# Performance work log

Measured on AMD Instinct MI355X. Metric: run time of the kernel, lower is better.

Reference implementation:

```python
import jax, jax.numpy as jnp
import numpy as np
import math

DIM_EMB = 1024
KSQRT = math.sqrt(DIM_EMB)


def setup_inputs() -> dict:
    key = jax.random.key(0)
    ks = jax.random.split(key, 7)
    b, t, e, d = 4, 4096, DIM_EMB, 1024
    s = 1.0 / math.sqrt(e)
    return {
        "x": jax.random.normal(ks[0], (b, t, e), dtype=jnp.float32),
        "Wq": jax.random.normal(ks[1], (d, e), dtype=jnp.float32) * s,
        "bq": jax.random.normal(ks[2], (d,), dtype=jnp.float32) * s,
        "Wk": jax.random.normal(ks[3], (d, e), dtype=jnp.float32) * s,
        "bk": jax.random.normal(ks[4], (d,), dtype=jnp.float32) * s,
        "Wv": jax.random.normal(ks[5], (d, e), dtype=jnp.float32) * s,
        "bv": jax.random.normal(ks[6], (d,), dtype=jnp.float32) * s,
    }


def reference(x, Wq, bq, Wk, bk, Wv, bv):
    # Linear projections: x [b,t,e] @ W.T [e,d] + b
    q = jnp.einsum('bte,de->btd', x, Wq) + bq
    k = jnp.einsum('bte,de->btd', x, Wk) + bk
    v = jnp.einsum('bte,de->btd', x, Wv) + bv
    # scaled dot-product attention, scale = sqrt(dim_emb) per source
    dot = jnp.einsum('bqd,bkd->bqk', q, k) / KSQRT
    p = jax.nn.softmax(dot, axis=-1)  # dim=2 == last axis for 3D tensor
    z = jnp.einsum('bqk,bkd->bqd', p, v)
    return z
```

## Files before the change

kernel.cpp:

```cpp
#include <hip/hip_runtime.h>
#include <hip/hip_bf16.h>

typedef __bf16 bf16x8 __attribute__((ext_vector_type(8)));
typedef float  f32x4  __attribute__((ext_vector_type(4)));

typedef __attribute__((address_space(1))) const void* as1p;
typedef __attribute__((address_space(3))) void*       as3p;

__device__ __forceinline__ void gl16(const void* g, void* l) {
    __builtin_amdgcn_global_load_lds((as1p)g, (as3p)l, 16, 0, 0);
}
#define MEMFENCE asm volatile("" ::: "memory")
#define BARRIER  do { MEMFENCE; __builtin_amdgcn_s_barrier(); MEMFENCE; } while (0)

__global__ __launch_bounds__(256)
void cvt_f32_bf16(const float* __restrict__ in, __bf16* __restrict__ out, long n8)
{
    long i = (long)blockIdx.x * blockDim.x + threadIdx.x;
    const long stride = (long)gridDim.x * blockDim.x;
    for (; i < n8; i += stride) {
        f32x4 a = ((const f32x4*)in)[2*i];
        f32x4 b = ((const f32x4*)in)[2*i + 1];
        bf16x8 o;
        #pragma unroll
        for (int j = 0; j < 4; ++j) { o[j] = (__bf16)a[j]; o[4+j] = (__bf16)b[j]; }
        ((bf16x8*)out)[i] = o;
    }
}

__global__ __launch_bounds__(256)
void pack_bias(const float* __restrict__ a, const float* __restrict__ b,
               const float* __restrict__ c, float* __restrict__ o)
{
    int i = blockIdx.x * 256 + threadIdx.x;
    const float* s = (i < 1024) ? a : (i < 2048) ? b : c;
    o[i] = s[i & 1023];
}

__global__ __launch_bounds__(256)
void prepass(const float* __restrict__ x,
             const float* __restrict__ Wq, const float* __restrict__ Wk,
             const float* __restrict__ Wv,
             const float* __restrict__ bq, const float* __restrict__ bk,
             const float* __restrict__ bv,
             __bf16* __restrict__ wall, __bf16* __restrict__ xb,
             float* __restrict__ bp)
{
    const long NW8 = 393216;
    const long NX8 = 2097152;
    long tid0 = (long)blockIdx.x * blockDim.x + threadIdx.x;
    if (tid0 < 3072) {
        const float* s = (tid0 < 1024) ? bq : (tid0 < 2048) ? bk : bv;
        bp[tid0] = s[tid0 & 1023];
    }
    const long stride = (long)gridDim.x * blockDim.x;
    for (long i = tid0; i < NW8 + NX8; i += stride) {
        const float* src;
        __bf16* dst;
        if (i < NW8) {
            int w = (int)(i >> 17);
            long off8 = i & 131071;
            src = ((w == 0) ? Wq : (w == 1) ? Wk : Wv) + off8 * 8;
            dst = wall + i * 8;
        } else {
            long j8 = i - NW8;
            src = x + j8 * 8;
            dst = xb + j8 * 8;
        }
        f32x4 a = ((const f32x4*)src)[0];
        f32x4 b = ((const f32x4*)src)[1];
        bf16x8 o;
        #pragma unroll
        for (int j = 0; j < 4; ++j) { o[j] = (__bf16)a[j]; o[4+j] = (__bf16)b[j]; }
        *(bf16x8*)dst = o;
    }
}

template<int EPI>
__global__ __launch_bounds__(512, 2)
void gemm8p(const __bf16* __restrict__ A, const __bf16* __restrict__ B,
            void* __restrict__ C0, void* __restrict__ C1,
            const float* __restrict__ aux, float* __restrict__ psum,
            int ldA, int ldB, int ldC, int Ktiles,
            long szA, long szB, long szC, long szAux, long szPsum,
            int nkz, float alpha)
{
    __shared__ char lds[163840];

    const int tid  = threadIdx.x;
    const int wave = tid >> 6, lane = tid & 63;
    const int wm = wave >> 2, wn = wave & 3;
    const int rl = lane & 15, kg = lane >> 4;
    const int z  = blockIdx.z;

    const __bf16* Ab = A + (long)z * ((EPI == 0) ? 0 : szA);
    const __bf16* Bb = B + (long)z * szB;

    const int P     = tid * 16;
    const int srow  = P >> 7;
    const int scolb = (P & 127) ^ ((srow & 7) << 4);
    const long rbA = (long)ldA * 2;
    const long rbB = (long)ldB * 2;
    const char* gA = (const char*)Ab + ((long)blockIdx.x * 256 + srow) * rbA + scolb;
    const char* gB = (const char*)Bb + ((long)blockIdx.y * 256 + srow) * rbB + scolb;

    auto stageA = [&](int buf, int h, int kt) {
        const char* s = gA + (long)h * 128 * rbA + (long)kt * 128;
        char* d = lds + buf * 32768 + h * 16384 + wave * 1024;
        gl16(s, d);
        gl16(s + 64 * rbA, d + 8192);
    };
    auto stageB = [&](int buf, int h, int kt) {
        const char* s = gB + (long)h * 128 * rbB + (long)kt * 128;
        char* d = lds + 98304 + buf * 32768 + h * 16384 + wave * 1024;
        gl16(s, d);
        gl16(s + 64 * rbB, d + 8192);
    };

    const int csw[2] = { (kg << 4) ^ ((rl & 7) << 4),
                         ((kg << 4) ^ ((rl & 7) << 4)) ^ 64 };
    const int aoff = wm * 16384 + rl * 128;
    const int boff = (wn >> 1) * 16384 + ((wn & 1) * 64 + rl) * 128;

    stageA(0, 0, 0); stageA(0, 1, 0);
    stageB(0, 0, 0); stageB(0, 1, 0);
    if (Ktiles > 1) {
        stageA(1, 0, 1); stageA(1, 1, 1);
        asm volatile("s_waitcnt vmcnt(4)" ::: "memory");
    } else {
        asm volatile("s_waitcnt vmcnt(0)" ::: "memory");
    }
    BARRIER;

    f32x4 acc[8][4] = {};
    int ab = 0, bb = 0, as_ = 2;

    for (int t = 0; t < Ktiles; ++t) {
        const char* rA = lds + ab * 32768;
        const char* rB = lds + 98304 + bb * 32768;
        const int sbb = bb ^ 1;
        bf16x8 a[4][2], b[4][2];

        #pragma unroll
        for (int mi = 0; mi < 4; ++mi)
            #pragma unroll
            for (int ks = 0; ks < 2; ++ks)
                a[mi][ks] = *(const bf16x8*)(rA + aoff + mi * 2048 + csw[ks]);
        #pragma unroll
        for (int ni = 0; ni < 4; ++ni)
            #pragma unroll
            for (int ks = 0; ks < 2; ++ks)
                b[ni][ks] = *(const bf16x8*)(rB + boff + ni * 2048 + csw[ks]);
        if (t + 1 < Ktiles) { stageB(sbb, 0, t + 1); stageB(sbb, 1, t + 1); }

        __builtin_amdgcn_s_setprio(1);
        #pragma unroll
        for (int mi = 0; mi < 4; ++mi)
            #pragma unroll
            for (int ni = 0; ni < 4; ++ni)
                #pragma unroll
                for (int ks = 0; ks < 2; ++ks)
                    acc[mi][ni] = __builtin_amdgcn_mfma_f32_16x16x32_bf16(
                        a[mi][ks], b[ni][ks], acc[mi][ni], 0, 0, 0);
        __builtin_amdgcn_s_setprio(0);

        #pragma unroll
        for (int mi = 0; mi < 4; ++mi)
            #pragma unroll
            for (int ks = 0; ks < 2; ++ks)
                a[mi][ks] = *(const bf16x8*)(rA + aoff + (4 + mi) * 2048 + csw[ks]);
        if (t + 2 < Ktiles) { stageA(as_, 0, t + 2); stageA(as_, 1, t + 2); }

        __builtin_amdgcn_s_setprio(1);
        #pragma unroll
        for (int mi = 0; mi < 4; ++mi)
            #pragma unroll
            for (int ni = 0; ni < 4; ++ni)
                #pragma unroll
                for (int ks = 0; ks < 2; ++ks)
                    acc[4 + mi][ni] = __builtin_amdgcn_mfma_f32_16x16x32_bf16(
                        a[mi][ks], b[ni][ks], acc[4 + mi][ni], 0, 0, 0);
        __builtin_amdgcn_s_setprio(0);

        if (t + 2 < Ktiles)      asm volatile("s_waitcnt vmcnt(4)" ::: "memory");
        else if (t + 1 < Ktiles) asm volatile("s_waitcnt vmcnt(0)" ::: "memory");
        if (t + 1 < Ktiles) BARRIER;

        ab = (ab == 2) ? 0 : ab + 1;
        bb ^= 1;
        as_ = (as_ == 2) ? 0 : as_ + 1;
    }

    const int rowg = blockIdx.x * 256 + wm * 128 + kg * 4;
    const int colg = blockIdx.y * 256 + wn * 64 + rl;

    if (EPI == 0) {
        __bf16* C = (__bf16*)C0 + (long)z * szC;
        const float* bbv = aux + (long)z * szAux;
        float bv[4];
        #pragma unroll
        for (int ni = 0; ni < 4; ++ni) bv[ni] = bbv[colg + ni * 16];
        #pragma unroll
        for (int mi = 0; mi < 8; ++mi)
            #pragma unroll
            for (int j = 0; j < 4; ++j) {
                __bf16* cr = C + (long)(rowg + mi * 16 + j) * ldC + colg;
                #pragma unroll
                for (int ni = 0; ni < 4; ++ni)
                    cr[ni * 16] = (__bf16)(acc[mi][ni][j] + bv[ni]);
            }
    } else if (EPI == 1) {
        BARRIER;
        __bf16* C = (__bf16*)C0 + (long)z * szC;
        float* wsum = (float*)lds;
        float rsm[8][4];
        #pragma unroll
        for (int mi = 0; mi < 8; ++mi)
            #pragma unroll
            for (int j = 0; j < 4; ++j) {
                float s = 0.f;
                __bf16* cr = C + (long)(rowg + mi * 16 + j) * ldC + colg;
                #pragma unroll
                for (int ni = 0; ni < 4; ++ni) {
                    float e = __expf(acc[mi][ni][j] * alpha);
                    cr[ni * 16] = (__bf16)e;
                    s += e;
                }
                rsm[mi][j] = s;
            }
        #pragma unroll
        for (int mi = 0; mi < 8; ++mi)
            #pragma unroll
            for (int j = 0; j < 4; ++j) {
                float s = rsm[mi][j];
                s += __shfl_xor(s, 1); s += __shfl_xor(s, 2);
                s += __shfl_xor(s, 4); s += __shfl_xor(s, 8);
                rsm[mi][j] = s;
            }
        if (rl == 0) {
            #pragma unroll
            for (int mi = 0; mi < 8; ++mi)
                #pragma unroll
                for (int j = 0; j < 4; ++j)
                    wsum[wn * 256 + wm * 128 + mi * 16 + kg * 4 + j] = rsm[mi][j];
        }
        __syncthreads();
        if (tid < 256) {
            float s = wsum[tid] + wsum[256 + tid] + wsum[512 + tid] + wsum[768 + tid];
            psum[(long)z * szPsum + (long)blockIdx.y * 4096 + blockIdx.x * 256 + tid] = s;
        }
    } else if (EPI == 2) {
        float* C = (float*)C0 + (long)z * szC;
        const float* rs = aux + (long)z * szAux;
        #pragma unroll
        for (int mi = 0; mi < 8; ++mi)
            #pragma unroll
            for (int j = 0; j < 4; ++j) {
                int r = rowg + mi * 16 + j;
                float inv = 1.f / rs[r];
                float* cr = C + (long)r * ldC + colg;
                #pragma unroll
                for (int ni = 0; ni < 4; ++ni) cr[ni * 16] = acc[mi][ni][j] * inv;
            }
    } else {
        float* C = (z < nkz - 1) ? ((float*)C0 + (long)z * szC) : (float*)C1;
        #pragma unroll
        for (int mi = 0; mi < 8; ++mi)
            #pragma unroll
            for (int j = 0; j < 4; ++j) {
                float* cr = C + (long)(rowg + mi * 16 + j) * ldC + colg;
                #pragma unroll
                for (int ni = 0; ni < 4; ++ni) cr[ni * 16] = acc[mi][ni][j];
            }
    }
}

__global__ __launch_bounds__(256)
void transpose64(const __bf16* __restrict__ in, __bf16* __restrict__ out,
                 int T, int D, long sIn, long sOut)
{
    __shared__ __bf16 tile[64][72];
    const __bf16* pin  = in  + (long)blockIdx.z * sIn;
    __bf16*       pout = out + (long)blockIdx.z * sOut;
    const int t0 = blockIdx.x * 64, d0 = blockIdx.y * 64;
    const int tid = threadIdx.x;
    const int rr = tid >> 3;
    const int cc = (tid & 7) * 8;

    #pragma unroll
    for (int it = 0; it < 2; ++it) {
        int r = rr + it * 32;
        bf16x8 v = *(const bf16x8*)(pin + (long)(t0 + r) * D + d0 + cc);
        *(bf16x8*)&tile[r][cc] = v;
    }
    __syncthreads();
    #pragma unroll
    for (int it = 0; it < 2; ++it) {
        int dr = rr + it * 32;
        bf16x8 o;
        #pragma unroll
        for (int j = 0; j < 8; ++j) o[j] = tile[cc + j][dr];
        *(bf16x8*)(pout + (long)(d0 + dr) * T + t0 + cc) = o;
    }
}

__global__ __launch_bounds__(256)
void rowsum16(const float* __restrict__ psum, float* __restrict__ rs)
{
    int i = blockIdx.x * 256 + threadIdx.x;
    int b = i >> 12, r = i & 4095;
    const float* p = psum + (long)b * 65536 + r;
    float s = 0.f;
    #pragma unroll
    for (int cb = 0; cb < 16; ++cb) s += p[cb * 4096];
    rs[i] = s;
}

__global__ __launch_bounds__(256)
void pv_reduce(float* __restrict__ outb, const float* __restrict__ parts,
               int np, const float* __restrict__ rs)
{
    long i = ((long)blockIdx.x * 256 + threadIdx.x) * 4;
    f32x4 v = *(f32x4*)(outb + i);
    for (int p = 0; p < np; ++p)
        v += *(const f32x4*)(parts + (long)p * 4194304 + i);
    float inv = 1.f / rs[i >> 10];
    v *= inv;
    *(f32x4*)(outb + i) = v;
}

extern "C" void kernel_launch(void* const* d_in, const int* in_sizes, int n_in,
                              void* d_out, int out_size, void* d_ws, size_t ws_size,
                              hipStream_t stream)
{
    const float* x  = (const float*)d_in[0];
    const float* Wq = (const float*)d_in[1];
    const float* bq = (const float*)d_in[2];
    const float* Wk = (const float*)d_in[3];
    const float* bk = (const float*)d_in[4];
    const float* Wv = (const float*)d_in[5];
    const float* bv = (const float*)d_in[6];
    float* out = (float*)d_out;

    const long T = 4096, E = 1024, D = 1024;
    const long TD = T * D;
    const long TT = T * T;
    const long WB = D * E;
    const float ALPHA = 1.0f / 32.0f;
    char* W = (char*)d_ws;

    const size_t need_A2 = 236007424;
    const size_t need_B2 = 191131648;

    if (ws_size >= need_A2) {
        __bf16* q    = (__bf16*)(W);
        __bf16* k    = (__bf16*)(W + 33554432);
        __bf16* vtmp = (__bf16*)(W + 67108864);
        __bf16* P    = (__bf16*)(W + 100663296);
        __bf16* xb   = (__bf16*)(W + 100663296);
        __bf16* wall = (__bf16*)(W + 134217728);
        __bf16* vt   = (__bf16*)(W);
        float*  psum = (float*) (W + 234881024);
        float*  rs   = (float*) (W + 235929600);
        float*  bp   = (float*) (W + 235995136);

        prepass<<<4096, 256, 0, stream>>>(x, Wq, Wk, Wv, bq, bk, bv, wall, xb, bp);

        gemm8p<0><<<dim3(64,4,3), 512, 0, stream>>>(
            xb, wall, q, nullptr, bp, nullptr,
            1024, 1024, 1024, 16, 0, WB, 4*TD, 1024, 0, 0, 0.f);

        gemm8p<1><<<dim3(16,16,4), 512, 0, stream>>>(
            q, k, P, nullptr, nullptr, psum,
            1024, 1024, 4096, 16, TD, TD, TT, 0, 65536, 0, ALPHA);

        transpose64<<<dim3(64,16,4), 256, 0, stream>>>(vtmp, vt, (int)T, (int)D, TD, TD);

        rowsum16<<<64, 256, 0, stream>>>(psum, rs);

        gemm8p<2><<<dim3(16,4,4), 512, 0, stream>>>(
            P, vt, out, nullptr, rs, nullptr,
            4096, 4096, 1024, 64, TT, TD, TD, 4096, 0, 0, 0.f);
    } else if (ws_size >= need_B2) {
        __bf16* wall  = (__bf16*)(W);
        __bf16* xb    = (__bf16*)(W + 6291456);
        float*  parts = (float*) (W + 6291456);
        __bf16* vt    = (__bf16*)(W + 56623104);
        __bf16* q     = (__bf16*)(W + 90177536);
        __bf16* k     = (__bf16*)(W + 123731968);
        __bf16* P     = (__bf16*)(W + 157286400);
        float*  psum  = (float*) (W + 190840832);
        float*  rs    = (float*) (W + 191102976);
        float*  bp    = (float*) (W + 191119360);

        prepass<<<4096, 256, 0, stream>>>(x, Wq, Wk, Wv, bq, bk, bv, wall, xb, bp);

        gemm8p<0><<<dim3(64,4,3), 512, 0, stream>>>(
            xb, wall, q, nullptr, bp, nullptr,
            1024, 1024, 1024, 16, 0, WB, 4*TD, 1024, 0, 0, 0.f);

        transpose64<<<dim3(64,16,4), 256, 0, stream>>>(P, vt, (int)T, (int)D, TD, TD);

        for (int b = 0; b < 4; ++b) {
            gemm8p<1><<<dim3(16,16,1), 512, 0, stream>>>(
                q + b*TD, k + b*TD, P, nullptr, nullptr, psum,
                1024, 1024, 4096, 16, 0, 0, 0, 0, 0, 0, ALPHA);
            rowsum16<<<16, 256, 0, stream>>>(psum, rs);
            gemm8p<3><<<dim3(16,4,4), 512, 0, stream>>>(
                P, vt + b*TD, parts, out + b*TD, nullptr, nullptr,
                4096, 4096, 1024, 16, 1024, 1024, TD, 0, 0, 4, 0.f);
            pv_reduce<<<4096, 256, 0, stream>>>(out + b*TD, parts, 3, rs);
        }
    } else {
        __bf16* wall  = (__bf16*)(W);
        __bf16* xb    = (__bf16*)(W + 6291456);
        float*  parts = (float*) (W + 6291456);
        __bf16* q     = (__bf16*)(W + 14680064);
        __bf16* k     = (__bf16*)(W + 23068672);
        __bf16* vt    = (__bf16*)(W + 31457280);
        __bf16* P     = (__bf16*)(W + 39845888);
        float*  psum  = (float*) (W + 73400320);
        float*  rs    = (float*) (W + 73662464);
        float*  bp    = (float*) (W + 73678848);

        pack_bias<<<12, 256, 0, stream>>>(bq, bk, bv, bp);
        cvt_f32_bf16<<<512, 256, 0, stream>>>(Wq, wall, WB/8);
        cvt_f32_bf16<<<512, 256, 0, stream>>>(Wk, wall + WB, WB/8);
        cvt_f32_bf16<<<512, 256, 0, stream>>>(Wv, wall + 2*WB, WB/8);

        for (int b = 0; b < 4; ++b) {
            cvt_f32_bf16<<<2048, 256, 0, stream>>>(x + b*TD, xb, TD/8);
            gemm8p<0><<<dim3(16,4,1), 512, 0, stream>>>(
                xb, wall, q, nullptr, bp, nullptr,
                1024, 1024, 1024, 16, 0, 0, 0, 0, 0, 0, 0.f);
            gemm8p<0><<<dim3(16,4,1), 512, 0, stream>>>(
                xb, wall + WB, k, nullptr, bp + 1024, nullptr,
                1024, 1024, 1024, 16, 0, 0, 0, 0, 0, 0, 0.f);
            gemm8p<0><<<dim3(16,4,1), 512, 0, stream>>>(
                xb, wall + 2*WB, P, nullptr, bp + 2048, nullptr,
                1024, 1024, 1024, 16, 0, 0, 0, 0, 0, 0, 0.f);
            transpose64<<<dim3(64,16,1), 256, 0, stream>>>(P, vt, (int)T, (int)D, 0, 0);
            gemm8p<1><<<dim3(16,16,1), 512, 0, stream>>>(
                q, k, P, nullptr, nullptr, psum,
                1024, 1024, 4096, 16, 0, 0, 0, 0, 0, 0, ALPHA);
            rowsum16<<<16, 256, 0, stream>>>(psum, rs);
            gemm8p<3><<<dim3(16,4,2), 512, 0, stream>>>(
                P, vt, parts, out + b*TD, nullptr, nullptr,
                4096, 4096, 1024, 32, 2048, 2048, TD, 0, 0, 2, 0.f);
            pv_reduce<<<4096, 256, 0, stream>>>(out + b*TD, parts, 1, rs);
        }
    }
}
```

Baseline: 402.0 us.

## Add four-phase barrier-synchronised MFMA schedule for the QKV projection GEMM

Adds a template schedule parameter to the GEMM. The new schedule splits each K-tile into four MFMA quarters, each preceded by partial LDS fragment loads, one staged global load, a barrier and an lgkmcnt wait. It is used only for the QKV projection on the large-workspace path. The default schedule also drops its s_setprio hints, which affects the QK and PV GEMMs. The aim is finer overlap of memory staging with matrix math across waves, at the cost of many more barriers per iteration.

New measurement: 412.1 us. 2.5% more time.

```diff
diff --git a/kernel.cpp b/kernel.cpp
--- a/kernel.cpp
+++ b/kernel.cpp
@@ -12,6 +12,7 @@
 }
 #define MEMFENCE asm volatile("" ::: "memory")
 #define BARRIER  do { MEMFENCE; __builtin_amdgcn_s_barrier(); MEMFENCE; } while (0)
+#define LGKM0    asm volatile("s_waitcnt lgkmcnt(0)" ::: "memory")
 
 __global__ __launch_bounds__(256)
 void cvt_f32_bf16(const float* __restrict__ in, __bf16* __restrict__ out, long n8)
@@ -76,7 +77,7 @@
     }
 }
 
-template<int EPI>
+template<int EPI, int SCHED = 0>
 __global__ __launch_bounds__(512, 2)
 void gemm8p(const __bf16* __restrict__ A, const __bf16* __restrict__ B,
             void* __restrict__ C0, void* __restrict__ C1,
@@ -141,50 +142,125 @@
         const int sbb = bb ^ 1;
         bf16x8 a[4][2], b[4][2];
 
-        #pragma unroll
-        for (int mi = 0; mi < 4; ++mi)
-            #pragma unroll
-            for (int ks = 0; ks < 2; ++ks)
-                a[mi][ks] = *(const bf16x8*)(rA + aoff + mi * 2048 + csw[ks]);
-        #pragma unroll
-        for (int ni = 0; ni < 4; ++ni)
-            #pragma unroll
-            for (int ks = 0; ks < 2; ++ks)
-                b[ni][ks] = *(const bf16x8*)(rB + boff + ni * 2048 + csw[ks]);
-        if (t + 1 < Ktiles) { stageB(sbb, 0, t + 1); stageB(sbb, 1, t + 1); }
-
-        __builtin_amdgcn_s_setprio(1);
-        #pragma unroll
-        for (int mi = 0; mi < 4; ++mi)
+        if constexpr (SCHED == 0) {
+            #pragma unroll
+            for (int mi = 0; mi < 4; ++mi)
+                #pragma unroll
+                for (int ks = 0; ks < 2; ++ks)
+                    a[mi][ks] = *(const bf16x8*)(rA + aoff + mi * 2048 + csw[ks]);
             #pragma unroll
             for (int ni = 0; ni < 4; ++ni)
                 #pragma unroll
                 for (int ks = 0; ks < 2; ++ks)
-                    acc[mi][ni] = __builtin_amdgcn_mfma_f32_16x16x32_bf16(
-                        a[mi][ks], b[ni][ks], acc[mi][ni], 0, 0, 0);
-        __builtin_amdgcn_s_setprio(0);
-
-        #pragma unroll
-        for (int mi = 0; mi < 4; ++mi)
-            #pragma unroll
-            for (int ks = 0; ks < 2; ++ks)
-                a[mi][ks] = *(const bf16x8*)(rA + aoff + (4 + mi) * 2048 + csw[ks]);
-        if (t + 2 < Ktiles) { stageA(as_, 0, t + 2); stageA(as_, 1, t + 2); }
-
-        __builtin_amdgcn_s_setprio(1);
-        #pragma unroll
-        for (int mi = 0; mi < 4; ++mi)
-            #pragma unroll
-            for (int ni = 0; ni < 4; ++ni)
-                #pragma unroll
-                for (int ks = 0; ks < 2; ++ks)
-                    acc[4 + mi][ni] = __builtin_amdgcn_mfma_f32_16x16x32_bf16(
-                        a[mi][ks], b[ni][ks], acc[4 + mi][ni], 0, 0, 0);
-        __builtin_amdgcn_s_setprio(0);
-
-        if (t + 2 < Ktiles)      asm volatile("s_waitcnt vmcnt(4)" ::: "memory");
-        else if (t + 1 < Ktiles) asm volatile("s_waitcnt vmcnt(0)" ::: "memory");
-        if (t + 1 < Ktiles) BARRIER;
+                    b[ni][ks] = *(const bf16x8*)(rB + boff + ni * 2048 + csw[ks]);
+            if (t + 1 < Ktiles) { stageB(sbb, 0, t + 1); stageB(sbb, 1, t + 1); }
+
+            #pragma unroll
+            for (int mi = 0; mi < 4; ++mi)
+                #pragma unroll
+                for (int ni = 0; ni < 4; ++ni)
+                    #pragma unroll
+                    for (int ks = 0; ks < 2; ++ks)
+                        acc[mi][ni] = __builtin_amdgcn_mfma_f32_16x16x32_bf16(
+                            a[mi][ks], b[ni][ks], acc[mi][ni], 0, 0, 0);
+
+            #pragma unroll
+            for (int mi = 0; mi < 4; ++mi)
+                #pragma unroll
+                for (int ks = 0; ks < 2; ++ks)
+                    a[mi][ks] = *(const bf16x8*)(rA + aoff + (4 + mi) * 2048 + csw[ks]);
+            if (t + 2 < Ktiles) { stageA(as_, 0, t + 2); stageA(as_, 1, t + 2); }
+
+            #pragma unroll
+            for (int mi = 0; mi < 4; ++mi)
+                #pragma unroll
+                for (int ni = 0; ni < 4; ++ni)
+                    #pragma unroll
+                    for (int ks = 0; ks < 2; ++ks)
+                        acc[4 + mi][ni] = __builtin_amdgcn_mfma_f32_16x16x32_bf16(
+                            a[mi][ks], b[ni][ks], acc[4 + mi][ni], 0, 0, 0);
+
+            if (t + 2 < Ktiles)      asm volatile("s_waitcnt vmcnt(4)" ::: "memory");
+            else if (t + 1 < Ktiles) asm volatile("s_waitcnt vmcnt(0)" ::: "memory");
+            if (t + 1 < Ktiles) BARRIER;
+        } else {
+            #pragma unroll
+            for (int mi = 0; mi < 4; ++mi)
+                #pragma unroll
+                for (int ks = 0; ks < 2; ++ks)
+                    a[mi][ks] = *(const bf16x8*)(rA + aoff + mi * 2048 + csw[ks]);
+            #pragma unroll
+            for (int ni = 0; ni < 2; ++ni)
+                #pragma unroll
+                for (int ks = 0; ks < 2; ++ks)
+                    b[ni][ks] = *(const bf16x8*)(rB + boff + ni * 2048 + csw[ks]);
+            if (t + 1 < Ktiles) stageB(sbb, 0, t + 1);
+            BARRIER; LGKM0;
+            __builtin_amdgcn_s_setprio(1);
+            #pragma unroll
+            for (int mi = 0; mi < 4; ++mi)
+                #pragma unroll
+                for (int ni = 0; ni < 2; ++ni)
+                    #pragma unroll
+                    for (int ks = 0; ks < 2; ++ks)
+                        acc[mi][ni] = __builtin_amdgcn_mfma_f32_16x16x32_bf16(
+                            a[mi][ks], b[ni][ks], acc[mi][ni], 0, 0, 0);
+            __builtin_amdgcn_s_setprio(0);
+            BARRIER;
+
+            #pragma unroll
+            for (int ni = 2; ni < 4; ++ni)
+                #pragma unroll
+                for (int ks = 0; ks < 2; ++ks)
+                    b[ni][ks] = *(const bf16x8*)(rB + boff + ni * 2048 + csw[ks]);
+            if (t + 1 < Ktiles) stageB(sbb, 1, t + 1);
+            BARRIER; LGKM0;
+            __builtin_amdgcn_s_setprio(1);
+            #pragma unroll
+            for (int mi = 0; mi < 4; ++mi)
+                #pragma unroll
+                for (int ni = 2; ni < 4; ++ni)
+                    #pragma unroll
+                    for (int ks = 0; ks < 2; ++ks)
+                        acc[mi][ni] = __builtin_amdgcn_mfma_f32_16x16x32_bf16(
+                            a[mi][ks], b[ni][ks], acc[mi][ni], 0, 0, 0);
+            __builtin_amdgcn_s_setprio(0);
+            BARRIER;
+
+            #pragma unroll
+            for (int mi = 0; mi < 4; ++mi)
+                #pragma unroll
+                for (int ks = 0; ks < 2; ++ks)
+                    a[mi][ks] = *(const bf16x8*)(rA + aoff + (4 + mi) * 2048 + csw[ks]);
+            if (t + 2 < Ktiles) stageA(as_, 0, t + 2);
+            BARRIER; LGKM0;
+            __builtin_amdgcn_s_setprio(1);
+            #pragma unroll
+            for (int mi = 0; mi < 4; ++mi)
+                #pragma unroll
+                for (int ni = 0; ni < 2; ++ni)
+                    #pragma unroll
+                    for (int ks = 0; ks < 2; ++ks)
+                        acc[4 + mi][ni] = __builtin_amdgcn_mfma_f32_16x16x32_bf16(
+                            a[mi][ks], b[ni][ks], acc[4 + mi][ni], 0, 0, 0);
+            __builtin_amdgcn_s_setprio(0);
+            BARRIER;
+
+            if (t + 2 < Ktiles) stageA(as_, 1, t + 2);
+            __builtin_amdgcn_s_setprio(1);
+            #pragma unroll
+            for (int mi = 0; mi < 4; ++mi)
+                #pragma unroll
+                for (int ni = 2; ni < 4; ++ni)
+                    #pragma unroll
+                    for (int ks = 0; ks < 2; ++ks)
+                        acc[4 + mi][ni] = __builtin_amdgcn_mfma_f32_16x16x32_bf16(
+                            a[mi][ks], b[ni][ks], acc[4 + mi][ni], 0, 0, 0);
+            __builtin_amdgcn_s_setprio(0);
+            if (t + 2 < Ktiles)      asm volatile("s_waitcnt vmcnt(4)" ::: "memory");
+            else if (t + 1 < Ktiles) asm volatile("s_waitcnt vmcnt(0)" ::: "memory");
+            if (t + 1 < Ktiles) BARRIER;
+        }
 
         ab = (ab == 2) ? 0 : ab + 1;
         bb ^= 1;
@@ -366,11 +442,11 @@
 
         prepass<<<4096, 256, 0, stream>>>(x, Wq, Wk, Wv, bq, bk, bv, wall, xb, bp);
 
-        gemm8p<0><<<dim3(64,4,3), 512, 0, stream>>>(
+        gemm8p<0, 1><<<dim3(64,4,3), 512, 0, stream>>>(
             xb, wall, q, nullptr, bp, nullptr,
             1024, 1024, 1024, 16, 0, WB, 4*TD, 1024, 0, 0, 0.f);
 
-        gemm8p<1><<<dim3(16,16,4), 512, 0, stream>>>(
+        gemm8p<1, 0><<<dim3(16,16,4), 512, 0, stream>>>(
             q, k, P, nullptr, nullptr, psum,
             1024, 1024, 4096, 16, TD, TD, TT, 0, 65536, 0, ALPHA);
 
@@ -378,7 +454,7 @@
 
         rowsum16<<<64, 256, 0, stream>>>(psum, rs);
 
-        gemm8p<2><<<dim3(16,4,4), 512, 0, stream>>>(
+        gemm8p<2, 0><<<dim3(16,4,4), 512, 0, stream>>>(
             P, vt, out, nullptr, rs, nullptr,
             4096, 4096, 1024, 64, TT, TD, TD, 4096, 0, 0, 0.f);
     } else if (ws_size >= need_B2) {
@@ -395,18 +471,18 @@
 
         prepass<<<4096, 256, 0, stream>>>(x, Wq, Wk, Wv, bq, bk, bv, wall, xb, bp);
 
-        gemm8p<0><<<dim3(64,4,3), 512, 0, stream>>>(
+        gemm8p<0, 0><<<dim3(64,4,3), 512, 0, stream>>>(
             xb, wall, q, nullptr, bp, nullptr,
             1024, 1024, 1024, 16, 0, WB, 4*TD, 1024, 0, 0, 0.f);
 
         transpose64<<<dim3(64,16,4), 256, 0, stream>>>(P, vt, (int)T, (int)D, TD, TD);
 
         for (int b = 0; b < 4; ++b) {
-            gemm8p<1><<<dim3(16,16,1), 512, 0, stream>>>(
+            gemm8p<1, 0><<<dim3(16,16,1), 512, 0, stream>>>(
                 q + b*TD, k + b*TD, P, nullptr, nullptr, psum,
                 1024, 1024, 4096, 16, 0, 0, 0, 0, 0, 0, ALPHA);
             rowsum16<<<16, 256, 0, stream>>>(psum, rs);
-            gemm8p<3><<<dim3(16,4,4), 512, 0, stream>>>(
+            gemm8p<3, 0><<<dim3(16,4,4), 512, 0, stream>>>(
                 P, vt + b*TD, parts, out + b*TD, nullptr, nullptr,
                 4096, 4096, 1024, 16, 1024, 1024, TD, 0, 0, 4, 0.f);
             pv_reduce<<<4096, 256, 0, stream>>>(out + b*TD, parts, 3, rs);
@@ -430,21 +506,21 @@
 
         for (int b = 0; b < 4; ++b) {
             cvt_f32_bf16<<<2048, 256, 0, stream>>>(x + b*TD, xb, TD/8);
-            gemm8p<0><<<dim3(16,4,1), 512, 0, stream>>>(
+            gemm8p<0, 0><<<dim3(16,4,1), 512, 0, stream>>>(
                 xb, wall, q, nullptr, bp, nullptr,
                 1024, 1024, 1024, 16, 0, 0, 0, 0, 0, 0, 0.f);
-            gemm8p<0><<<dim3(16,4,1), 512, 0, stream>>>(
+            gemm8p<0, 0><<<dim3(16,4,1), 512, 0, stream>>>(
                 xb, wall + WB, k, nullptr, bp + 1024, nullptr,
                 1024, 1024, 1024, 16, 0, 0, 0, 0, 0, 0, 0.f);
-            gemm8p<0><<<dim3(16,4,1), 512, 0, stream>>>(
+            gemm8p<0, 0><<<dim3(16,4,1), 512, 0, stream>>>(
                 xb, wall + 2*WB, P, nullptr, bp + 2048, nullptr,
                 1024, 1024, 1024, 16, 0, 0, 0, 0, 0, 0, 0.f);
             transpose64<<<dim3(64,16,1), 256, 0, stream>>>(P, vt, (int)T, (int)D, 0, 0);
-            gemm8p<1><<<dim3(16,16,1), 512, 0, stream>>>(
+            gemm8p<1, 0><<<dim3(16,16,1), 512, 0, stream>>>(
                 q, k, P, nullptr, nullptr, psum,
                 1024, 1024, 4096, 16, 0, 0, 0, 0, 0, 0, ALPHA);
             rowsum16<<<16, 256, 0, stream>>>(psum, rs);
-            gemm8p<3><<<dim3(16,4,2), 512, 0, stream>>>(
+            gemm8p<3, 0><<<dim3(16,4,2), 512, 0, stream>>>(
                 P, vt, parts, out + b*TD, nullptr, nullptr,
                 4096, 4096, 1024, 32, 2048, 2048, TD, 0, 0, 2, 0.f);
             pv_reduce<<<4096, 256, 0, stream>>>(out + b*TD, parts, 1, rs);
```
